# Kernel optimization log

Hardware: AMD Instinct MI355X
Metric: run time of the kernel (lower is better)

The kernel has to match this reference:

```python
import jax, jax.numpy as jnp
import numpy as np

D = 768
H = 12
HD = D // H  # 64
EPS = 1e-12


def setup_inputs() -> dict:
    key = jax.random.key(0)
    ks = jax.random.split(key, 9)
    B, S = 4, 2048
    s = 1.0 / np.sqrt(D)
    inp = {
        "hidden_states": jax.random.normal(ks[0], (B, S, D), dtype=jnp.float32),
        "Wq": jax.random.normal(ks[1], (D, D), dtype=jnp.float32) * s,
        "bq": jnp.zeros((D,), dtype=jnp.float32),
        "Wk": jax.random.normal(ks[2], (D, D), dtype=jnp.float32) * s,
        "bk": jnp.zeros((D,), dtype=jnp.float32),
        "Wv": jax.random.normal(ks[3], (D, D), dtype=jnp.float32) * s,
        "bv": jnp.zeros((D,), dtype=jnp.float32),
        "Wo": jax.random.normal(ks[4], (D, D), dtype=jnp.float32) * s,
        "bo": jnp.zeros((D,), dtype=jnp.float32),
    }
    return inp


def _heads(x):
    # [B,S,D] -> [B,H,S,HD]
    B, S, _ = x.shape
    return x.reshape(B, S, H, HD).transpose(0, 2, 1, 3)


def reference(hidden_states, Wq, bq, Wk, bk, Wv, bv, Wo, bo):
    q = _heads(hidden_states @ Wq.T + bq)
    k = _heads(hidden_states @ Wk.T + bk)
    v = _heads(hidden_states @ Wv.T + bv)
    # NOTE: original code does NOT scale by 1/sqrt(head_dim)
    scores = jnp.einsum("bhqd,bhkd->bhqk", q, k)
    probs = jax.nn.softmax(scores, axis=-1)
    ctx = jnp.einsum("bhqk,bhkd->bhqd", probs, v)
    B, _, S, _ = ctx.shape
    ctx = ctx.transpose(0, 2, 1, 3).reshape(B, S, D)
    # output dense + residual
    h = ctx @ Wo.T + bo + hidden_states
    # custom LayerNorm: unbiased std, divide by (std + eps), no affine applied
    mean = jnp.mean(h, axis=-1, keepdims=True)
    std = jnp.sqrt(jnp.var(h, axis=-1, keepdims=True, ddof=1))
    return (h - mean) / (std + EPS)
```

## Files before the change

kernel.cpp:

```cpp
#include <hip/hip_runtime.h>

typedef unsigned short u16;
typedef unsigned int   u32;
typedef __attribute__((ext_vector_type(4))) u32    u32x4;
typedef __attribute__((ext_vector_type(4))) u16    u16x4;
typedef __attribute__((ext_vector_type(8))) u16    u16x8;
typedef __attribute__((ext_vector_type(8))) __bf16 bf16x8;
typedef __attribute__((ext_vector_type(4))) float  f32x4;

#define LOG2E 1.4426950408889634f

__device__ __forceinline__ float bf2f(u16 x) {
    u32 u = ((u32)x) << 16;
    return __builtin_bit_cast(float, u);
}
__device__ __forceinline__ u16 f2bf(float f) {
    u32 u = __builtin_bit_cast(u32, f);
    return (u16)((u + 0x7FFFu + ((u >> 16) & 1u)) >> 16);
}
__device__ __forceinline__ u32 pk2(float a, float b) {
#if __has_builtin(__builtin_amdgcn_cvt_pk_bf16_f32)
    return __builtin_bit_cast(u32, __builtin_amdgcn_cvt_pk_bf16_f32(a, b));
#else
    return (u32)f2bf(a) | ((u32)f2bf(b) << 16);
#endif
}
__device__ __forceinline__ u16x4 pack4(f32x4 v) {
    u32 lo = pk2(v[0], v[1]), hi = pk2(v[2], v[3]);
    u32 both[2] = {lo, hi};
    return __builtin_bit_cast(u16x4, *(unsigned long long*)both);
}
__device__ __forceinline__ float fexp2(float x) {
#if __has_builtin(__builtin_amdgcn_exp2f)
    return __builtin_amdgcn_exp2f(x);
#else
    float r;
    asm("v_exp_f32 %0, %1" : "=v"(r) : "v"(x));
    return r;
#endif
}
__device__ __forceinline__ bf16x8 ldfrag(const u16* p) {
    return __builtin_bit_cast(bf16x8, *(const u32x4*)p);
}

__global__ __launch_bounds__(256) void convert(
    const float* __restrict__ X,
    const float* __restrict__ Wq, const float* __restrict__ Wk,
    const float* __restrict__ Wv, const float* __restrict__ Wo,
    u16* __restrict__ Xb, u16* __restrict__ Wqb, u16* __restrict__ Wkb,
    u16* __restrict__ Wvb, u16* __restrict__ Wob)
{
    const int NX = 1572864;
    const int NW = 147456;
    int i = blockIdx.x * 256 + threadIdx.x;
    const float* src; u16* dst; int off; float sc = 1.0f;
    if (i < NX)               { src = X;  dst = Xb;  off = i; }
    else if (i < NX + NW)     { src = Wq; dst = Wqb; off = i - NX; sc = LOG2E; }
    else if (i < NX + 2 * NW) { src = Wk; dst = Wkb; off = i - NX - NW; }
    else if (i < NX + 3 * NW) { src = Wv; dst = Wvb; off = i - NX - 2 * NW; }
    else                      { src = Wo; dst = Wob; off = i - NX - 3 * NW; }
    f32x4 v = *(const f32x4*)&src[(size_t)off * 4];
    f32x4 s4 = {sc, sc, sc, sc};
    v *= s4;
    *(u16x4*)&dst[(size_t)off * 4] = pack4(v);
}

__global__ __launch_bounds__(256) void gemm_qkv(
    const u16* __restrict__ Xb, const u16* __restrict__ Wcat,
    const float* __restrict__ bq, const float* __restrict__ bk, const float* __restrict__ bv,
    u16* __restrict__ Qo, u16* __restrict__ Ko, u16* __restrict__ Vt)
{
    __shared__ __align__(16) u16 sA[128 * 72];
    __shared__ __align__(16) u16 sB[128 * 72];

    const int tid  = threadIdx.x;
    const int wave = tid >> 6, lane = tid & 63;
    const int quad = lane >> 4, l16 = lane & 15;
    const int wr = wave >> 1, wc = wave & 1;
    const int m0 = blockIdx.x * 128;
    const int ny = blockIdx.y;
    const int which = ny / 6;
    const int n0 = ny * 128;
    const int n_in = (ny % 6) * 128;

    int rr[4], cc[4];
#pragma unroll
    for (int p = 0; p < 4; ++p) { int c = p * 256 + tid; rr[p] = c >> 3; cc[p] = (c & 7) * 8; }

    f32x4 acc[4][4] = {};
    u32x4 ra[4], rb[4];
#pragma unroll
    for (int p = 0; p < 4; ++p) {
        ra[p] = *(const u32x4*)&Xb  [(size_t)(m0 + rr[p]) * 768 + cc[p]];
        rb[p] = *(const u32x4*)&Wcat[(size_t)(n0 + rr[p]) * 768 + cc[p]];
    }

    for (int k0 = 0; k0 < 768; k0 += 64) {
        __syncthreads();
#pragma unroll
        for (int p = 0; p < 4; ++p) {
            *(u32x4*)&sA[rr[p] * 72 + cc[p]] = ra[p];
            *(u32x4*)&sB[rr[p] * 72 + cc[p]] = rb[p];
        }
        int kn = k0 + 64; if (kn == 768) kn = 0;
#pragma unroll
        for (int p = 0; p < 4; ++p) {
            ra[p] = *(const u32x4*)&Xb  [(size_t)(m0 + rr[p]) * 768 + kn + cc[p]];
            rb[p] = *(const u32x4*)&Wcat[(size_t)(n0 + rr[p]) * 768 + kn + cc[p]];
        }
        __syncthreads();

#pragma unroll
        for (int ks = 0; ks < 2; ++ks) {
            bf16x8 af[4], bfr[4];
#pragma unroll
            for (int i = 0; i < 4; ++i)
                af[i] = ldfrag(&sA[(wr * 64 + i * 16 + l16) * 72 + ks * 32 + quad * 8]);
#pragma unroll
            for (int j = 0; j < 4; ++j)
                bfr[j] = ldfrag(&sB[(wc * 64 + j * 16 + l16) * 72 + ks * 32 + quad * 8]);
#pragma unroll
            for (int i = 0; i < 4; ++i)
#pragma unroll
                for (int j = 0; j < 4; ++j)
                    acc[i][j] = __builtin_amdgcn_mfma_f32_16x16x32_bf16(af[i], bfr[j], acc[i][j], 0, 0, 0);
        }
    }

    const float* bias = (which == 0) ? bq : ((which == 1) ? bk : bv);
    if (which < 2) {
        u16* out = (which == 0) ? Qo : Ko;
        const float scale = (which == 0) ? LOG2E : 1.0f;
#pragma unroll
        for (int j = 0; j < 4; ++j) {
            int n = n_in + wc * 64 + j * 16 + l16;
            float bvv = bias[n] * scale;
            int h = n >> 6, hd = n & 63;
#pragma unroll
            for (int i = 0; i < 4; ++i) {
#pragma unroll
                for (int r = 0; r < 4; ++r) {
                    int m = m0 + wr * 64 + i * 16 + quad * 4 + r;
                    int b = m >> 11, s = m & 2047;
                    out[(((size_t)(b * 12 + h) * 2048) + s) * 64 + hd] =
                        f2bf(acc[i][j][r] + bvv);
                }
            }
        }
    } else {
#pragma unroll
        for (int j = 0; j < 4; ++j) {
            int n = n_in + wc * 64 + j * 16 + l16;
            float bvv = bias[n];
            int h = n >> 6, hd = n & 63;
            f32x4 b4 = {bvv, bvv, bvv, bvv};
#pragma unroll
            for (int i = 0; i < 4; ++i) {
                int m = m0 + wr * 64 + i * 16 + quad * 4;
                int b = m >> 11, s = m & 2047;
                *(u16x4*)&Vt[((size_t)(b * 12 + h) * 64 + hd) * 2048 + s] = pack4(acc[i][j] + b4);
            }
        }
    }
}

__global__ __launch_bounds__(256, 3) void attn(
    const u16* __restrict__ Q, const u16* __restrict__ K, const u16* __restrict__ Vt,
    u16* __restrict__ ctx)
{
    const int bid = blockIdx.x;
    const int xcd = bid & 7, slot = bid >> 3;
    const int bh = xcd * 6 + (slot % 6);
    const int q0 = (slot / 6) * 128;
    const int b = bh / 12, h = bh % 12;
    const u16* Qb  = Q  + (size_t)bh * (2048 * 64);
    const u16* Kb  = K  + (size_t)bh * (2048 * 64);
    const u16* Vtb = Vt + (size_t)bh * (64 * 2048);

    __shared__ __align__(16) u16 sK [64 * 72];
    __shared__ __align__(16) u16 sVt[64 * 72];
    __shared__ __align__(16) u16 sPt[128 * 72];

    const int tid = threadIdx.x;
    const int wave = tid >> 6, lane = tid & 63;
    const int quad = lane >> 4, l16 = lane & 15;

    const int kr0 = tid >> 3,           kc0 = (tid & 7) * 8;
    const int kr1 = (256 + tid) >> 3,   kc1 = ((256 + tid) & 7) * 8;

    bf16x8 qf[2][2];
#pragma unroll
    for (int jn = 0; jn < 2; ++jn)
#pragma unroll
        for (int ks = 0; ks < 2; ++ks)
            qf[jn][ks] = ldfrag(&Qb[(size_t)(q0 + wave * 32 + jn * 16 + l16) * 64 + ks * 32 + quad * 8]);

    bf16x8 vones;
    {
        u16x8 o;
#pragma unroll
        for (int t = 0; t < 8; ++t) o[t] = 0x3F80;
        vones = __builtin_bit_cast(bf16x8, o);
    }

    f32x4 oacc[2][4] = {};
    f32x4 Lacc[2] = {};

    u32x4 rk0, rk1, rv0, rv1;
    rk0 = *(const u32x4*)&Kb [(size_t)kr0 * 64 + kc0];
    rk1 = *(const u32x4*)&Kb [(size_t)kr1 * 64 + kc1];
    rv0 = *(const u32x4*)&Vtb[(size_t)kr0 * 2048 + kc0];
    rv1 = *(const u32x4*)&Vtb[(size_t)kr1 * 2048 + kc1];

    for (int kt = 0; kt < 2048; kt += 64) {
        __syncthreads();
        *(u32x4*)&sK [kr0 * 72 + kc0] = rk0;
        *(u32x4*)&sK [kr1 * 72 + kc1] = rk1;
        *(u32x4*)&sVt[kr0 * 72 + kc0] = rv0;
        *(u32x4*)&sVt[kr1 * 72 + kc1] = rv1;
        int ktn = (kt + 64) & 2047;
        rk0 = *(const u32x4*)&Kb [(size_t)(ktn + kr0) * 64 + kc0];
        rk1 = *(const u32x4*)&Kb [(size_t)(ktn + kr1) * 64 + kc1];
        rv0 = *(const u32x4*)&Vtb[(size_t)kr0 * 2048 + ktn + kc0];
        rv1 = *(const u32x4*)&Vtb[(size_t)kr1 * 2048 + ktn + kc1];
        __syncthreads();

        f32x4 sacc[4][2] = {};
#pragma unroll
        for (int ks = 0; ks < 2; ++ks) {
            bf16x8 kf[4];
#pragma unroll
            for (int i = 0; i < 4; ++i)
                kf[i] = ldfrag(&sK[(i * 16 + l16) * 72 + ks * 32 + quad * 8]);
#pragma unroll
            for (int i = 0; i < 4; ++i)
#pragma unroll
                for (int jn = 0; jn < 2; ++jn)
                    sacc[i][jn] = __builtin_amdgcn_mfma_f32_16x16x32_bf16(kf[i], qf[jn][ks], sacc[i][jn], 0, 0, 0);
        }

#pragma unroll
        for (int i = 0; i < 4; ++i) {
#pragma unroll
            for (int jn = 0; jn < 2; ++jn) {
                f32x4 pe;
#pragma unroll
                for (int r = 0; r < 4; ++r) pe[r] = fexp2(sacc[i][jn][r]);
                *(u16x4*)&sPt[(wave * 32 + jn * 16 + l16) * 72 + i * 16 + quad * 4] = pack4(pe);
            }
        }

#pragma unroll
        for (int ks2 = 0; ks2 < 2; ++ks2) {
            bf16x8 pf[2], vf[4];
#pragma unroll
            for (int jn = 0; jn < 2; ++jn)
                pf[jn] = ldfrag(&sPt[(wave * 32 + jn * 16 + l16) * 72 + ks2 * 32 + quad * 8]);
#pragma unroll
            for (int jh = 0; jh < 4; ++jh)
                vf[jh] = ldfrag(&sVt[(jh * 16 + l16) * 72 + ks2 * 32 + quad * 8]);
#pragma unroll
            for (int jn = 0; jn < 2; ++jn) {
#pragma unroll
                for (int jh = 0; jh < 4; ++jh)
                    oacc[jn][jh] = __builtin_amdgcn_mfma_f32_16x16x32_bf16(pf[jn], vf[jh], oacc[jn][jh], 0, 0, 0);
                Lacc[jn] = __builtin_amdgcn_mfma_f32_16x16x32_bf16(pf[jn], vones, Lacc[jn], 0, 0, 0);
            }
        }
    }

#pragma unroll
    for (int jn = 0; jn < 2; ++jn) {
#pragma unroll
        for (int r = 0; r < 4; ++r) {
            float linv = 1.0f / Lacc[jn][r];
            int srow = q0 + wave * 32 + jn * 16 + quad * 4 + r;
            size_t rowbase = ((size_t)(b * 2048 + srow)) * 768 + h * 64;
#pragma unroll
            for (int jh = 0; jh < 4; ++jh)
                ctx[rowbase + jh * 16 + l16] = f2bf(oacc[jn][jh][r] * linv);
        }
    }
}

__global__ __launch_bounds__(256) void gemm_out(
    const u16* __restrict__ A,
    const u16* __restrict__ Wob,
    const float* __restrict__ bo,
    const float* __restrict__ X,
    u16* __restrict__ Hout)
{
    __shared__ __align__(16) u16 sA[128 * 72];
    __shared__ __align__(16) u16 sB[128 * 72];

    const int tid = threadIdx.x;
    const int wave = tid >> 6, lane = tid & 63;
    const int quad = lane >> 4, l16 = lane & 15;
    const int wr = wave >> 1, wc = wave & 1;
    const int m0 = blockIdx.x * 128, n0 = blockIdx.y * 128;

    int rr[4], cc[4];
#pragma unroll
    for (int p = 0; p < 4; ++p) { int c = p * 256 + tid; rr[p] = c >> 3; cc[p] = (c & 7) * 8; }

    f32x4 acc[4][4] = {};
    u32x4 ra[4], rb[4];
#pragma unroll
    for (int p = 0; p < 4; ++p) {
        ra[p] = *(const u32x4*)&A  [(size_t)(m0 + rr[p]) * 768 + cc[p]];
        rb[p] = *(const u32x4*)&Wob[(size_t)(n0 + rr[p]) * 768 + cc[p]];
    }

    for (int k0 = 0; k0 < 768; k0 += 64) {
        __syncthreads();
#pragma unroll
        for (int p = 0; p < 4; ++p) {
            *(u32x4*)&sA[rr[p] * 72 + cc[p]] = ra[p];
            *(u32x4*)&sB[rr[p] * 72 + cc[p]] = rb[p];
        }
        int kn = k0 + 64; if (kn == 768) kn = 0;
#pragma unroll
        for (int p = 0; p < 4; ++p) {
            ra[p] = *(const u32x4*)&A  [(size_t)(m0 + rr[p]) * 768 + kn + cc[p]];
            rb[p] = *(const u32x4*)&Wob[(size_t)(n0 + rr[p]) * 768 + kn + cc[p]];
        }
        __syncthreads();

#pragma unroll
        for (int ks = 0; ks < 2; ++ks) {
            bf16x8 af[4], bfr[4];
#pragma unroll
            for (int i = 0; i < 4; ++i)
                af[i] = ldfrag(&sA[(wr * 64 + i * 16 + l16) * 72 + ks * 32 + quad * 8]);
#pragma unroll
            for (int j = 0; j < 4; ++j)
                bfr[j] = ldfrag(&sB[(wc * 64 + j * 16 + l16) * 72 + ks * 32 + quad * 8]);
#pragma unroll
            for (int i = 0; i < 4; ++i)
#pragma unroll
                for (int j = 0; j < 4; ++j)
                    acc[i][j] = __builtin_amdgcn_mfma_f32_16x16x32_bf16(af[i], bfr[j], acc[i][j], 0, 0, 0);
        }
    }

#pragma unroll
    for (int j = 0; j < 4; ++j) {
        int n = n0 + wc * 64 + j * 16 + l16;
        float bv_ = bo[n];
#pragma unroll
        for (int i = 0; i < 4; ++i) {
#pragma unroll
            for (int r = 0; r < 4; ++r) {
                size_t m = m0 + wr * 64 + i * 16 + quad * 4 + r;
                Hout[m * 768 + n] = f2bf(acc[i][j][r] + bv_ + X[m * 768 + n]);
            }
        }
    }
}

__global__ __launch_bounds__(256) void lnorm(const u16* __restrict__ Hs, float* __restrict__ out)
{
    const int row = blockIdx.x;
    const u16* hr = Hs + (size_t)row * 768;
    const int tid = threadIdx.x;
    float v0 = bf2f(hr[tid]), v1 = bf2f(hr[tid + 256]), v2 = bf2f(hr[tid + 512]);
    float s = v0 + v1 + v2;
    float ss = v0 * v0 + v1 * v1 + v2 * v2;
#pragma unroll
    for (int off = 1; off < 64; off <<= 1) {
        s  += __shfl_xor(s, off);
        ss += __shfl_xor(ss, off);
    }
    __shared__ float red[8];
    const int wave = tid >> 6, lane = tid & 63;
    if (lane == 0) { red[wave] = s; red[4 + wave] = ss; }
    __syncthreads();
    s  = red[0] + red[1] + red[2] + red[3];
    ss = red[4] + red[5] + red[6] + red[7];
    float mean = s * (1.0f / 768.0f);
    float var = fmaxf((ss - 768.0f * mean * mean) * (1.0f / 767.0f), 0.0f);
    float inv = 1.0f / (sqrtf(var) + 1e-12f);
    float* orow = out + (size_t)row * 768;
    orow[tid]       = (v0 - mean) * inv;
    orow[tid + 256] = (v1 - mean) * inv;
    orow[tid + 512] = (v2 - mean) * inv;
}

extern "C" void kernel_launch(void* const* d_in, const int* in_sizes, int n_in,
                              void* d_out, int out_size, void* d_ws, size_t ws_size,
                              hipStream_t stream)
{
    const float* X  = (const float*)d_in[0];
    const float* Wq = (const float*)d_in[1];
    const float* bq = (const float*)d_in[2];
    const float* Wk = (const float*)d_in[3];
    const float* bk = (const float*)d_in[4];
    const float* Wv = (const float*)d_in[5];
    const float* bv = (const float*)d_in[6];
    const float* Wo = (const float*)d_in[7];
    const float* bo = (const float*)d_in[8];
    float* out = (float*)d_out;

    const size_t TE = (size_t)8192 * 768;
    const size_t WN = (size_t)768 * 768;
    u16* ws  = (u16*)d_ws;
    u16* Xb  = ws;
    u16* Qw  = ws + TE;
    u16* Kw  = ws + 2 * TE;
    u16* Vt  = ws + 3 * TE;
    u16* Wqb = ws + 4 * TE;
    u16* Wkb = Wqb + WN;
    u16* Wvb = Wqb + 2 * WN;
    u16* Wob = Wqb + 3 * WN;
    u16* Cw  = Xb;
    u16* Hw  = Qw;

    convert<<<8448, 256, 0, stream>>>(X, Wq, Wk, Wv, Wo, Xb, Wqb, Wkb, Wvb, Wob);
    gemm_qkv<<<dim3(64, 18), 256, 0, stream>>>(Xb, Wqb, bq, bk, bv, Qw, Kw, Vt);
    attn<<<768, 256, 0, stream>>>(Qw, Kw, Vt, Cw);
    gemm_out<<<dim3(64, 6), 256, 0, stream>>>(Cw, Wob, bo, X, Hw);
    lnorm<<<8192, 256, 0, stream>>>(Hw, out);
}
```

Before: 238.3 us.

## Stage GEMM and attention tiles via direct global-to-LDS loads with double buffering

Replaces register-staged global loads followed by LDS stores with direct global_load_lds transfers into double-buffered, unpadded 32-wide LDS tiles, in both GEMMs and the attention K/V staging. This drops one barrier per iteration and the VGPR round trip. For Q/K the MFMA operands are swapped so the QKV epilogue can write four contiguous bf16 values per store instead of scalar stores. Risks include LDS bank conflicts from losing the padding, a smaller K step per iteration in the GEMMs, and no explicit wait for the async LDS loads before the barrier.

New measurement: 253.2 us. 1.06x slower.

```diff
diff --git a/kernel.cpp b/kernel.cpp
--- a/kernel.cpp
+++ b/kernel.cpp
@@ -41,6 +41,12 @@
 }
 __device__ __forceinline__ bf16x8 ldfrag(const u16* p) {
     return __builtin_bit_cast(bf16x8, *(const u32x4*)p);
+}
+__device__ __forceinline__ void g2l16(const u16* g, u16* l) {
+    __builtin_amdgcn_global_load_lds(
+        (const __attribute__((address_space(1))) u32*)g,
+        (__attribute__((address_space(3))) u32*)l,
+        16, 0, 0);
 }
 
 __global__ __launch_bounds__(256) void convert(
@@ -70,10 +76,10 @@
     const float* __restrict__ bq, const float* __restrict__ bk, const float* __restrict__ bv,
     u16* __restrict__ Qo, u16* __restrict__ Ko, u16* __restrict__ Vt)
 {
-    __shared__ __align__(16) u16 sA[128 * 72];
-    __shared__ __align__(16) u16 sB[128 * 72];
-
-    const int tid  = threadIdx.x;
+    __shared__ __align__(16) u16 sA[2][128 * 32];
+    __shared__ __align__(16) u16 sB[2][128 * 32];
+
+    const int tid = threadIdx.x;
     const int wave = tid >> 6, lane = tid & 63;
     const int quad = lane >> 4, l16 = lane & 15;
     const int wr = wave >> 1, wc = wave & 1;
@@ -83,42 +89,46 @@
     const int n0 = ny * 128;
     const int n_in = (ny % 6) * 128;
 
-    int rr[4], cc[4];
-#pragma unroll
-    for (int p = 0; p < 4; ++p) { int c = p * 256 + tid; rr[p] = c >> 3; cc[p] = (c & 7) * 8; }
+    const int drow = wave * 32 + (lane >> 2);
+    const int dcol = (lane & 3) * 8;
+    const u16* gA = &Xb  [(size_t)(m0 + drow) * 768 + dcol];
+    const u16* gB = &Wcat[(size_t)(n0 + drow) * 768 + dcol];
+    u16* lA = &sA[0][wave * 1024];
+    u16* lB = &sB[0][wave * 1024];
 
     f32x4 acc[4][4] = {};
-    u32x4 ra[4], rb[4];
-#pragma unroll
-    for (int p = 0; p < 4; ++p) {
-        ra[p] = *(const u32x4*)&Xb  [(size_t)(m0 + rr[p]) * 768 + cc[p]];
-        rb[p] = *(const u32x4*)&Wcat[(size_t)(n0 + rr[p]) * 768 + cc[p]];
-    }
-
-    for (int k0 = 0; k0 < 768; k0 += 64) {
+
+    g2l16(gA,            lA);
+    g2l16(gA + 16 * 768, lA + 512);
+    g2l16(gB,            lB);
+    g2l16(gB + 16 * 768, lB + 512);
+
+    for (int t = 0; t < 24; ++t) {
+        const int buf = t & 1;
         __syncthreads();
-#pragma unroll
-        for (int p = 0; p < 4; ++p) {
-            *(u32x4*)&sA[rr[p] * 72 + cc[p]] = ra[p];
-            *(u32x4*)&sB[rr[p] * 72 + cc[p]] = rb[p];
-        }
-        int kn = k0 + 64; if (kn == 768) kn = 0;
-#pragma unroll
-        for (int p = 0; p < 4; ++p) {
-            ra[p] = *(const u32x4*)&Xb  [(size_t)(m0 + rr[p]) * 768 + kn + cc[p]];
-            rb[p] = *(const u32x4*)&Wcat[(size_t)(n0 + rr[p]) * 768 + kn + cc[p]];
-        }
-        __syncthreads();
-
-#pragma unroll
-        for (int ks = 0; ks < 2; ++ks) {
-            bf16x8 af[4], bfr[4];
+        if (t < 23) {
+            const int k = (t + 1) * 32;
+            u16* dA = lA + (buf ^ 1) * 4096;
+            u16* dB = lB + (buf ^ 1) * 4096;
+            g2l16(gA + k,            dA);
+            g2l16(gA + k + 16 * 768, dA + 512);
+            g2l16(gB + k,            dB);
+            g2l16(gB + k + 16 * 768, dB + 512);
+        }
+        bf16x8 af[4], bfr[4];
+#pragma unroll
+        for (int i = 0; i < 4; ++i)
+            af[i] = ldfrag(&sA[buf][(wr * 64 + i * 16 + l16) * 32 + quad * 8]);
+#pragma unroll
+        for (int j = 0; j < 4; ++j)
+            bfr[j] = ldfrag(&sB[buf][(wc * 64 + j * 16 + l16) * 32 + quad * 8]);
+        if (which < 2) {
 #pragma unroll
             for (int i = 0; i < 4; ++i)
-                af[i] = ldfrag(&sA[(wr * 64 + i * 16 + l16) * 72 + ks * 32 + quad * 8]);
-#pragma unroll
-            for (int j = 0; j < 4; ++j)
-                bfr[j] = ldfrag(&sB[(wc * 64 + j * 16 + l16) * 72 + ks * 32 + quad * 8]);
+#pragma unroll
+                for (int j = 0; j < 4; ++j)
+                    acc[i][j] = __builtin_amdgcn_mfma_f32_16x16x32_bf16(bfr[j], af[i], acc[i][j], 0, 0, 0);
+        } else {
 #pragma unroll
             for (int i = 0; i < 4; ++i)
 #pragma unroll
@@ -130,21 +140,19 @@
     const float* bias = (which == 0) ? bq : ((which == 1) ? bk : bv);
     if (which < 2) {
         u16* out = (which == 0) ? Qo : Ko;
-        const float scale = (which == 0) ? LOG2E : 1.0f;
+        const float sc = (which == 0) ? LOG2E : 1.0f;
+        f32x4 sc4 = {sc, sc, sc, sc};
 #pragma unroll
         for (int j = 0; j < 4; ++j) {
-            int n = n_in + wc * 64 + j * 16 + l16;
-            float bvv = bias[n] * scale;
-            int h = n >> 6, hd = n & 63;
+            int nb = n_in + wc * 64 + j * 16 + quad * 4;
+            f32x4 b4 = *(const f32x4*)&bias[nb] * sc4;
+            int h = nb >> 6, hd0 = nb & 63;
 #pragma unroll
             for (int i = 0; i < 4; ++i) {
-#pragma unroll
-                for (int r = 0; r < 4; ++r) {
-                    int m = m0 + wr * 64 + i * 16 + quad * 4 + r;
-                    int b = m >> 11, s = m & 2047;
-                    out[(((size_t)(b * 12 + h) * 2048) + s) * 64 + hd] =
-                        f2bf(acc[i][j][r] + bvv);
-                }
+                int m = m0 + wr * 64 + i * 16 + l16;
+                int b = m >> 11, srow = m & 2047;
+                *(u16x4*)&out[(((size_t)(b * 12 + h) * 2048) + srow) * 64 + hd0] =
+                    pack4(acc[i][j] + b4);
             }
         }
     } else {
@@ -177,16 +185,16 @@
     const u16* Kb  = K  + (size_t)bh * (2048 * 64);
     const u16* Vtb = Vt + (size_t)bh * (64 * 2048);
 
-    __shared__ __align__(16) u16 sK [64 * 72];
-    __shared__ __align__(16) u16 sVt[64 * 72];
+    __shared__ __align__(16) u16 sK [2][2][64 * 32];
+    __shared__ __align__(16) u16 sVt[2][2][64 * 32];
     __shared__ __align__(16) u16 sPt[128 * 72];
 
     const int tid = threadIdx.x;
     const int wave = tid >> 6, lane = tid & 63;
     const int quad = lane >> 4, l16 = lane & 15;
 
-    const int kr0 = tid >> 3,           kc0 = (tid & 7) * 8;
-    const int kr1 = (256 + tid) >> 3,   kc1 = ((256 + tid) & 7) * 8;
+    const int drow = lane >> 2;
+    const int dcol = (lane & 3) * 8;
 
     bf16x8 qf[2][2];
 #pragma unroll
@@ -206,24 +214,25 @@
     f32x4 oacc[2][4] = {};
     f32x4 Lacc[2] = {};
 
-    u32x4 rk0, rk1, rv0, rv1;
-    rk0 = *(const u32x4*)&Kb [(size_t)kr0 * 64 + kc0];
-    rk1 = *(const u32x4*)&Kb [(size_t)kr1 * 64 + kc1];
-    rv0 = *(const u32x4*)&Vtb[(size_t)kr0 * 2048 + kc0];
-    rv1 = *(const u32x4*)&Vtb[(size_t)kr1 * 2048 + kc1];
+#pragma unroll
+    for (int p = 0; p < 2; ++p) {
+        g2l16(&Kb [(size_t)(wave * 16 + drow) * 64 + p * 32 + dcol],   &sK [0][p][wave * 512]);
+        g2l16(&Vtb[(size_t)(wave * 16 + drow) * 2048 + p * 32 + dcol], &sVt[0][p][wave * 512]);
+    }
 
     for (int kt = 0; kt < 2048; kt += 64) {
+        const int buf = (kt >> 6) & 1;
         __syncthreads();
-        *(u32x4*)&sK [kr0 * 72 + kc0] = rk0;
-        *(u32x4*)&sK [kr1 * 72 + kc1] = rk1;
-        *(u32x4*)&sVt[kr0 * 72 + kc0] = rv0;
-        *(u32x4*)&sVt[kr1 * 72 + kc1] = rv1;
-        int ktn = (kt + 64) & 2047;
-        rk0 = *(const u32x4*)&Kb [(size_t)(ktn + kr0) * 64 + kc0];
-        rk1 = *(const u32x4*)&Kb [(size_t)(ktn + kr1) * 64 + kc1];
-        rv0 = *(const u32x4*)&Vtb[(size_t)kr0 * 2048 + ktn + kc0];
-        rv1 = *(const u32x4*)&Vtb[(size_t)kr1 * 2048 + ktn + kc1];
-        __syncthreads();
+        if (kt + 64 < 2048) {
+            const int kn = kt + 64;
+#pragma unroll
+            for (int p = 0; p < 2; ++p) {
+                g2l16(&Kb [(size_t)(kn + wave * 16 + drow) * 64 + p * 32 + dcol],
+                      &sK [buf ^ 1][p][wave * 512]);
+                g2l16(&Vtb[(size_t)(wave * 16 + drow) * 2048 + kn + p * 32 + dcol],
+                      &sVt[buf ^ 1][p][wave * 512]);
+            }
+        }
 
         f32x4 sacc[4][2] = {};
 #pragma unroll
@@ -231,7 +240,7 @@
             bf16x8 kf[4];
 #pragma unroll
             for (int i = 0; i < 4; ++i)
-                kf[i] = ldfrag(&sK[(i * 16 + l16) * 72 + ks * 32 + quad * 8]);
+                kf[i] = ldfrag(&sK[buf][ks][(i * 16 + l16) * 32 + quad * 8]);
 #pragma unroll
             for (int i = 0; i < 4; ++i)
 #pragma unroll
@@ -258,7 +267,7 @@
                 pf[jn] = ldfrag(&sPt[(wave * 32 + jn * 16 + l16) * 72 + ks2 * 32 + quad * 8]);
 #pragma unroll
             for (int jh = 0; jh < 4; ++jh)
-                vf[jh] = ldfrag(&sVt[(jh * 16 + l16) * 72 + ks2 * 32 + quad * 8]);
+                vf[jh] = ldfrag(&sVt[buf][ks2][(jh * 16 + l16) * 32 + quad * 8]);
 #pragma unroll
             for (int jn = 0; jn < 2; ++jn) {
 #pragma unroll
@@ -290,8 +299,8 @@
     const float* __restrict__ X,
     u16* __restrict__ Hout)
 {
-    __shared__ __align__(16) u16 sA[128 * 72];
-    __shared__ __align__(16) u16 sB[128 * 72];
+    __shared__ __align__(16) u16 sA[2][128 * 32];
+    __shared__ __align__(16) u16 sB[2][128 * 32];
 
     const int tid = threadIdx.x;
     const int wave = tid >> 6, lane = tid & 63;
@@ -299,48 +308,44 @@
     const int wr = wave >> 1, wc = wave & 1;
     const int m0 = blockIdx.x * 128, n0 = blockIdx.y * 128;
 
-    int rr[4], cc[4];
-#pragma unroll
-    for (int p = 0; p < 4; ++p) { int c = p * 256 + tid; rr[p] = c >> 3; cc[p] = (c & 7) * 8; }
+    const int drow = wave * 32 + (lane >> 2);
+    const int dcol = (lane & 3) * 8;
+    const u16* gA = &A  [(size_t)(m0 + drow) * 768 + dcol];
+    const u16* gB = &Wob[(size_t)(n0 + drow) * 768 + dcol];
+    u16* lA = &sA[0][wave * 1024];
+    u16* lB = &sB[0][wave * 1024];
 
     f32x4 acc[4][4] = {};
-    u32x4 ra[4], rb[4];
-#pragma unroll
-    for (int p = 0; p < 4; ++p) {
-        ra[p] = *(const u32x4*)&A  [(size_t)(m0 + rr[p]) * 768 + cc[p]];
-        rb[p] = *(const u32x4*)&Wob[(size_t)(n0 + rr[p]) * 768 + cc[p]];
-    }
-
-    for (int k0 = 0; k0 < 768; k0 += 64) {
+
+    g2l16(gA,            lA);
+    g2l16(gA + 16 * 768, lA + 512);
+    g2l16(gB,            lB);
+    g2l16(gB + 16 * 768, lB + 512);
+
+    for (int t = 0; t < 24; ++t) {
+        const int buf = t & 1;
         __syncthreads();
-#pragma unroll
-        for (int p = 0; p < 4; ++p) {
-            *(u32x4*)&sA[rr[p] * 72 + cc[p]] = ra[p];
-            *(u32x4*)&sB[rr[p] * 72 + cc[p]] = rb[p];
-        }
-        int kn = k0 + 64; if (kn == 768) kn = 0;
-#pragma unroll
-        for (int p = 0; p < 4; ++p) {
-            ra[p] = *(const u32x4*)&A  [(size_t)(m0 + rr[p]) * 768 + kn + cc[p]];
-            rb[p] = *(const u32x4*)&Wob[(size_t)(n0 + rr[p]) * 768 + kn + cc[p]];
-        }
-        __syncthreads();
-
-#pragma unroll
-        for (int ks = 0; ks < 2; ++ks) {
-            bf16x8 af[4], bfr[4];
-#pragma unroll
-            for (int i = 0; i < 4; ++i)
-                af[i] = ldfrag(&sA[(wr * 64 + i * 16 + l16) * 72 + ks * 32 + quad * 8]);
+        if (t < 23) {
+            const int k = (t + 1) * 32;
+            u16* dA = lA + (buf ^ 1) * 4096;
+            u16* dB = lB + (buf ^ 1) * 4096;
+            g2l16(gA + k,            dA);
+            g2l16(gA + k + 16 * 768, dA + 512);
+            g2l16(gB + k,            dB);
+            g2l16(gB + k + 16 * 768, dB + 512);
+        }
+        bf16x8 af[4], bfr[4];
+#pragma unroll
+        for (int i = 0; i < 4; ++i)
+            af[i] = ldfrag(&sA[buf][(wr * 64 + i * 16 + l16) * 32 + quad * 8]);
+#pragma unroll
+        for (int j = 0; j < 4; ++j)
+            bfr[j] = ldfrag(&sB[buf][(wc * 64 + j * 16 + l16) * 32 + quad * 8]);
+#pragma unroll
+        for (int i = 0; i < 4; ++i)
 #pragma unroll
             for (int j = 0; j < 4; ++j)
-                bfr[j] = ldfrag(&sB[(wc * 64 + j * 16 + l16) * 72 + ks * 32 + quad * 8]);
-#pragma unroll
-            for (int i = 0; i < 4; ++i)
-#pragma unroll
-                for (int j = 0; j < 4; ++j)
-                    acc[i][j] = __builtin_amdgcn_mfma_f32_16x16x32_bf16(af[i], bfr[j], acc[i][j], 0, 0, 0);
-        }
+                acc[i][j] = __builtin_amdgcn_mfma_f32_16x16x32_bf16(af[i], bfr[j], acc[i][j], 0, 0, 0);
     }
 
 #pragma unroll
```

## Double-buffer attention K/V tiles via direct global-to-LDS loads with swizzle

Applied to the files above, without the earlier changes.

The attention kernel now loads K and V^T tiles with global_load_lds straight into double-buffered, XOR-swizzled shared memory, prefetching the next tile, and drops the second barrier per iteration. The QKV GEMM swaps MFMA operand order for Q/K so each lane holds four consecutive head-dim values, allowing vectorized bias loads and 8-byte stores. Shared-memory row padding in the GEMMs and the P tile changes from 72 to 80 elements. The aim is to remove register staging and a sync in the attention inner loop and to cut scalar scattered stores. In exchange the kernel depends on correct vmcnt handling for the LDS DMA, and the new padding may change LDS bank-conflict behaviour.

New measurement: 237.7 us. Within noise of the previous version (-0.3%).

```diff
diff --git a/kernel.cpp b/kernel.cpp
--- a/kernel.cpp
+++ b/kernel.cpp
@@ -41,6 +41,12 @@
 }
 __device__ __forceinline__ bf16x8 ldfrag(const u16* p) {
     return __builtin_bit_cast(bf16x8, *(const u32x4*)p);
+}
+__device__ __forceinline__ void g2l16(const u16* g, u16* l) {
+    __builtin_amdgcn_global_load_lds(
+        (const __attribute__((address_space(1))) u32*)g,
+        (__attribute__((address_space(3))) u32*)l,
+        16, 0, 0);
 }
 
 __global__ __launch_bounds__(256) void convert(
@@ -70,10 +76,10 @@
     const float* __restrict__ bq, const float* __restrict__ bk, const float* __restrict__ bv,
     u16* __restrict__ Qo, u16* __restrict__ Ko, u16* __restrict__ Vt)
 {
-    __shared__ __align__(16) u16 sA[128 * 72];
-    __shared__ __align__(16) u16 sB[128 * 72];
-
-    const int tid  = threadIdx.x;
+    __shared__ __align__(16) u16 sA[128 * 80];
+    __shared__ __align__(16) u16 sB[128 * 80];
+
+    const int tid = threadIdx.x;
     const int wave = tid >> 6, lane = tid & 63;
     const int quad = lane >> 4, l16 = lane & 15;
     const int wr = wave >> 1, wc = wave & 1;
@@ -99,8 +105,8 @@
         __syncthreads();
 #pragma unroll
         for (int p = 0; p < 4; ++p) {
-            *(u32x4*)&sA[rr[p] * 72 + cc[p]] = ra[p];
-            *(u32x4*)&sB[rr[p] * 72 + cc[p]] = rb[p];
+            *(u32x4*)&sA[rr[p] * 80 + cc[p]] = ra[p];
+            *(u32x4*)&sB[rr[p] * 80 + cc[p]] = rb[p];
         }
         int kn = k0 + 64; if (kn == 768) kn = 0;
 #pragma unroll
@@ -115,36 +121,42 @@
             bf16x8 af[4], bfr[4];
 #pragma unroll
             for (int i = 0; i < 4; ++i)
-                af[i] = ldfrag(&sA[(wr * 64 + i * 16 + l16) * 72 + ks * 32 + quad * 8]);
+                af[i] = ldfrag(&sA[(wr * 64 + i * 16 + l16) * 80 + ks * 32 + quad * 8]);
 #pragma unroll
             for (int j = 0; j < 4; ++j)
-                bfr[j] = ldfrag(&sB[(wc * 64 + j * 16 + l16) * 72 + ks * 32 + quad * 8]);
-#pragma unroll
-            for (int i = 0; i < 4; ++i)
-#pragma unroll
-                for (int j = 0; j < 4; ++j)
-                    acc[i][j] = __builtin_amdgcn_mfma_f32_16x16x32_bf16(af[i], bfr[j], acc[i][j], 0, 0, 0);
+                bfr[j] = ldfrag(&sB[(wc * 64 + j * 16 + l16) * 80 + ks * 32 + quad * 8]);
+            if (which < 2) {
+#pragma unroll
+                for (int i = 0; i < 4; ++i)
+#pragma unroll
+                    for (int j = 0; j < 4; ++j)
+                        acc[i][j] = __builtin_amdgcn_mfma_f32_16x16x32_bf16(bfr[j], af[i], acc[i][j], 0, 0, 0);
+            } else {
+#pragma unroll
+                for (int i = 0; i < 4; ++i)
+#pragma unroll
+                    for (int j = 0; j < 4; ++j)
+                        acc[i][j] = __builtin_amdgcn_mfma_f32_16x16x32_bf16(af[i], bfr[j], acc[i][j], 0, 0, 0);
+            }
         }
     }
 
     const float* bias = (which == 0) ? bq : ((which == 1) ? bk : bv);
     if (which < 2) {
         u16* out = (which == 0) ? Qo : Ko;
-        const float scale = (which == 0) ? LOG2E : 1.0f;
+        const float sc = (which == 0) ? LOG2E : 1.0f;
+        f32x4 sc4 = {sc, sc, sc, sc};
 #pragma unroll
         for (int j = 0; j < 4; ++j) {
-            int n = n_in + wc * 64 + j * 16 + l16;
-            float bvv = bias[n] * scale;
-            int h = n >> 6, hd = n & 63;
+            int nb = n_in + wc * 64 + j * 16 + quad * 4;
+            f32x4 b4 = *(const f32x4*)&bias[nb] * sc4;
+            int h = nb >> 6, hd0 = nb & 63;
 #pragma unroll
             for (int i = 0; i < 4; ++i) {
-#pragma unroll
-                for (int r = 0; r < 4; ++r) {
-                    int m = m0 + wr * 64 + i * 16 + quad * 4 + r;
-                    int b = m >> 11, s = m & 2047;
-                    out[(((size_t)(b * 12 + h) * 2048) + s) * 64 + hd] =
-                        f2bf(acc[i][j][r] + bvv);
-                }
+                int m = m0 + wr * 64 + i * 16 + l16;
+                int b = m >> 11, srow = m & 2047;
+                *(u16x4*)&out[(((size_t)(b * 12 + h) * 2048) + srow) * 64 + hd0] =
+                    pack4(acc[i][j] + b4);
             }
         }
     } else {
@@ -177,16 +189,17 @@
     const u16* Kb  = K  + (size_t)bh * (2048 * 64);
     const u16* Vtb = Vt + (size_t)bh * (64 * 2048);
 
-    __shared__ __align__(16) u16 sK [64 * 72];
-    __shared__ __align__(16) u16 sVt[64 * 72];
-    __shared__ __align__(16) u16 sPt[128 * 72];
+    __shared__ __align__(16) u16 sK [2][2][64 * 32];
+    __shared__ __align__(16) u16 sVt[2][2][64 * 32];
+    __shared__ __align__(16) u16 sPt[128 * 80];
 
     const int tid = threadIdx.x;
     const int wave = tid >> 6, lane = tid & 63;
     const int quad = lane >> 4, l16 = lane & 15;
 
-    const int kr0 = tid >> 3,           kc0 = (tid & 7) * 8;
-    const int kr1 = (256 + tid) >> 3,   kc1 = ((256 + tid) & 7) * 8;
+    const int drow = lane >> 2;
+    const int dcol = ((lane & 3) ^ ((lane >> 2) & 3)) * 8;
+    const int xq = (quad * 8) ^ ((l16 & 3) * 8);
 
     bf16x8 qf[2][2];
 #pragma unroll
@@ -206,24 +219,25 @@
     f32x4 oacc[2][4] = {};
     f32x4 Lacc[2] = {};
 
-    u32x4 rk0, rk1, rv0, rv1;
-    rk0 = *(const u32x4*)&Kb [(size_t)kr0 * 64 + kc0];
-    rk1 = *(const u32x4*)&Kb [(size_t)kr1 * 64 + kc1];
-    rv0 = *(const u32x4*)&Vtb[(size_t)kr0 * 2048 + kc0];
-    rv1 = *(const u32x4*)&Vtb[(size_t)kr1 * 2048 + kc1];
+#pragma unroll
+    for (int p = 0; p < 2; ++p) {
+        g2l16(&Kb [(size_t)(wave * 16 + drow) * 64 + p * 32 + dcol],   &sK [0][p][wave * 512]);
+        g2l16(&Vtb[(size_t)(wave * 16 + drow) * 2048 + p * 32 + dcol], &sVt[0][p][wave * 512]);
+    }
 
     for (int kt = 0; kt < 2048; kt += 64) {
+        const int buf = (kt >> 6) & 1;
         __syncthreads();
-        *(u32x4*)&sK [kr0 * 72 + kc0] = rk0;
-        *(u32x4*)&sK [kr1 * 72 + kc1] = rk1;
-        *(u32x4*)&sVt[kr0 * 72 + kc0] = rv0;
-        *(u32x4*)&sVt[kr1 * 72 + kc1] = rv1;
-        int ktn = (kt + 64) & 2047;
-        rk0 = *(const u32x4*)&Kb [(size_t)(ktn + kr0) * 64 + kc0];
-        rk1 = *(const u32x4*)&Kb [(size_t)(ktn + kr1) * 64 + kc1];
-        rv0 = *(const u32x4*)&Vtb[(size_t)kr0 * 2048 + ktn + kc0];
-        rv1 = *(const u32x4*)&Vtb[(size_t)kr1 * 2048 + ktn + kc1];
-        __syncthreads();
+        if (kt + 64 < 2048) {
+            const int kn = kt + 64;
+#pragma unroll
+            for (int p = 0; p < 2; ++p) {
+                g2l16(&Kb [(size_t)(kn + wave * 16 + drow) * 64 + p * 32 + dcol],
+                      &sK [buf ^ 1][p][wave * 512]);
+                g2l16(&Vtb[(size_t)(wave * 16 + drow) * 2048 + kn + p * 32 + dcol],
+                      &sVt[buf ^ 1][p][wave * 512]);
+            }
+        }
 
         f32x4 sacc[4][2] = {};
 #pragma unroll
@@ -231,7 +245,7 @@
             bf16x8 kf[4];
 #pragma unroll
             for (int i = 0; i < 4; ++i)
-                kf[i] = ldfrag(&sK[(i * 16 + l16) * 72 + ks * 32 + quad * 8]);
+                kf[i] = ldfrag(&sK[buf][ks][(i * 16 + l16) * 32 + xq]);
 #pragma unroll
             for (int i = 0; i < 4; ++i)
 #pragma unroll
@@ -246,7 +260,7 @@
                 f32x4 pe;
 #pragma unroll
                 for (int r = 0; r < 4; ++r) pe[r] = fexp2(sacc[i][jn][r]);
-                *(u16x4*)&sPt[(wave * 32 + jn * 16 + l16) * 72 + i * 16 + quad * 4] = pack4(pe);
+                *(u16x4*)&sPt[(wave * 32 + jn * 16 + l16) * 80 + i * 16 + quad * 4] = pack4(pe);
             }
         }
 
@@ -255,10 +269,10 @@
             bf16x8 pf[2], vf[4];
 #pragma unroll
             for (int jn = 0; jn < 2; ++jn)
-                pf[jn] = ldfrag(&sPt[(wave * 32 + jn * 16 + l16) * 72 + ks2 * 32 + quad * 8]);
+                pf[jn] = ldfrag(&sPt[(wave * 32 + jn * 16 + l16) * 80 + ks2 * 32 + quad * 8]);
 #pragma unroll
             for (int jh = 0; jh < 4; ++jh)
-                vf[jh] = ldfrag(&sVt[(jh * 16 + l16) * 72 + ks2 * 32 + quad * 8]);
+                vf[jh] = ldfrag(&sVt[buf][ks2][(jh * 16 + l16) * 32 + xq]);
 #pragma unroll
             for (int jn = 0; jn < 2; ++jn) {
 #pragma unroll
@@ -290,8 +304,8 @@
     const float* __restrict__ X,
     u16* __restrict__ Hout)
 {
-    __shared__ __align__(16) u16 sA[128 * 72];
-    __shared__ __align__(16) u16 sB[128 * 72];
+    __shared__ __align__(16) u16 sA[128 * 80];
+    __shared__ __align__(16) u16 sB[128 * 80];
 
     const int tid = threadIdx.x;
     const int wave = tid >> 6, lane = tid & 63;
@@ -315,8 +329,8 @@
         __syncthreads();
 #pragma unroll
         for (int p = 0; p < 4; ++p) {
-            *(u32x4*)&sA[rr[p] * 72 + cc[p]] = ra[p];
-            *(u32x4*)&sB[rr[p] * 72 + cc[p]] = rb[p];
+            *(u32x4*)&sA[rr[p] * 80 + cc[p]] = ra[p];
+            *(u32x4*)&sB[rr[p] * 80 + cc[p]] = rb[p];
         }
         int kn = k0 + 64; if (kn == 768) kn = 0;
 #pragma unroll
@@ -331,10 +345,10 @@
             bf16x8 af[4], bfr[4];
 #pragma unroll
             for (int i = 0; i < 4; ++i)
-                af[i] = ldfrag(&sA[(wr * 64 + i * 16 + l16) * 72 + ks * 32 + quad * 8]);
+                af[i] = ldfrag(&sA[(wr * 64 + i * 16 + l16) * 80 + ks * 32 + quad * 8]);
 #pragma unroll
             for (int j = 0; j < 4; ++j)
-                bfr[j] = ldfrag(&sB[(wc * 64 + j * 16 + l16) * 72 + ks * 32 + quad * 8]);
+                bfr[j] = ldfrag(&sB[(wc * 64 + j * 16 + l16) * 80 + ks * 32 + quad * 8]);
 #pragma unroll
             for (int i = 0; i < 4; ++i)
 #pragma unroll
```
